# Performance work log

Hardware: AMD Instinct MI355X
Metric: run time of the kernel (lower is better)

The kernel has to match this reference:

```python
import jax, jax.numpy as jnp
import numpy as np

K_SIGMA = 4.0  # self.k in the torch module


def setup_inputs() -> dict:
    key = jax.random.key(0)
    k1, k2, k3 = jax.random.split(key, 3)
    B, N = 4096, 16384
    output = jax.random.normal(k1, (B, N), dtype=jnp.float32)
    mean_grad = jax.random.normal(k2, (N,), dtype=jnp.float32)
    var_grad = jax.random.uniform(k3, (N,), dtype=jnp.float32)  # variance >= 0
    return {"output": output, "mean_grad": mean_grad, "var_grad": var_grad}


def _nan_checker(x):
    # replace NaN/Inf with 0, matching nan_checker()
    return jnp.where(jnp.isnan(x) | jnp.isinf(x), jnp.zeros((), x.dtype), x)


def reference(output, mean_grad, var_grad):
    # circular conv1d with kernel [-1, 1, 0] == x[i] - x[i-1] (circular shift-sub)
    x = _nan_checker(output)                      # [B, N]
    grad_y = x - jnp.roll(x, 1, axis=1)           # [B, N]
    std = jnp.sqrt(var_grad)                      # [N]
    lower = mean_grad - K_SIGMA * std             # [N]
    upper = mean_grad + K_SIGMA * std             # [N]
    mask = (grad_y < lower) | (grad_y > upper)    # [B, N] outlier mask
    return jnp.where(mask, jnp.zeros((), x.dtype), x)
```

## Files before the change

### kernel.cpp

```cpp
#include <hip/hip_runtime.h>


#define N_COLS 16384
#define COLS4  (N_COLS / 4)
#define COLS4_SHIFT 12
#define COLS4_MASK  (COLS4 - 1)

__device__ __forceinline__ float nan_clean(float v) {
    unsigned u = __float_as_uint(v);
    return ((u & 0x7f800000u) == 0x7f800000u) ? 0.0f : v;
}

__global__ __launch_bounds__(256) void correction_kernel(
    const float* __restrict__ x,
    const float* __restrict__ mean_grad,
    const float* __restrict__ var_grad,
    float* __restrict__ out)
{
    int t = blockIdx.x * blockDim.x + threadIdx.x;
    int row  = t >> COLS4_SHIFT;
    int col4 = t & COLS4_MASK;
    int j    = col4 << 2;
    long base = (long)row * N_COLS + j;

    float4 x4 = *(const float4*)(x + base);
    int jprev = (j + N_COLS - 1) & (N_COLS - 1);
    float prev = x[(long)row * N_COLS + jprev];

    float c0 = nan_clean(x4.x);
    float c1 = nan_clean(x4.y);
    float c2 = nan_clean(x4.z);
    float c3 = nan_clean(x4.w);
    float cp = nan_clean(prev);

    float4 m4 = *(const float4*)(mean_grad + j);
    float4 v4 = *(const float4*)(var_grad + j);

    float s0 = 4.0f * sqrtf(v4.x);
    float s1 = 4.0f * sqrtf(v4.y);
    float s2 = 4.0f * sqrtf(v4.z);
    float s3 = 4.0f * sqrtf(v4.w);

    float d0 = c0 - cp;
    float d1 = c1 - c0;
    float d2 = c2 - c1;
    float d3 = c3 - c2;

    float4 o;
    o.x = (d0 < m4.x - s0 || d0 > m4.x + s0) ? 0.0f : c0;
    o.y = (d1 < m4.y - s1 || d1 > m4.y + s1) ? 0.0f : c1;
    o.z = (d2 < m4.z - s2 || d2 > m4.z + s2) ? 0.0f : c2;
    o.w = (d3 < m4.w - s3 || d3 > m4.w + s3) ? 0.0f : c3;

    *(float4*)(out + base) = o;
}

extern "C" void kernel_launch(void* const* d_in, const int* in_sizes, int n_in,
                              void* d_out, int out_size, void* d_ws, size_t ws_size,
                              hipStream_t stream) {
    const float* x  = (const float*)d_in[0];
    const float* mg = (const float*)d_in[1];
    const float* vg = (const float*)d_in[2];
    float* out = (float*)d_out;

    int B = in_sizes[0] / N_COLS;
    long total_threads = (long)B * COLS4;
    int block = 256;
    int grid = (int)((total_threads + block - 1) / block);

    correction_kernel<<<grid, block, 0, stream>>>(x, mg, vg, out);
}
```

Measured before the change: 421.5 us.

## Process 32 rows per block and reuse per-column bounds across rows

Switches to a 2D grid where each block covers 1024 columns and 32 rows. Each thread computes the lower and upper bounds (sqrt and scaling) once and applies them to 32 rows, with four independent row loads in flight per loop iteration. This drops repeated mean/var loads and sqrt work per element and adds memory-level parallelism. In exchange there are far fewer blocks (16x128), and B must be a multiple of 32.

```diff
diff --git a/kernel.cpp b/kernel.cpp
--- a/kernel.cpp
+++ b/kernel.cpp
@@ -2,13 +2,35 @@
 
 
 #define N_COLS 16384
-#define COLS4  (N_COLS / 4)
-#define COLS4_SHIFT 12
-#define COLS4_MASK  (COLS4 - 1)
+#define N_MASK (N_COLS - 1)
+#define COLS_PER_BLOCK 1024
+#define ROWS_PER_BLOCK 32
 
 __device__ __forceinline__ float nan_clean(float v) {
     unsigned u = __float_as_uint(v);
     return ((u & 0x7f800000u) == 0x7f800000u) ? 0.0f : v;
+}
+
+struct Bounds { float lo0, hi0, lo1, hi1, lo2, hi2, lo3, hi3; };
+
+__device__ __forceinline__ float4 correct4(float4 a, float p, const Bounds& b) {
+    float c0 = nan_clean(a.x);
+    float c1 = nan_clean(a.y);
+    float c2 = nan_clean(a.z);
+    float c3 = nan_clean(a.w);
+    float cp = nan_clean(p);
+
+    float d0 = c0 - cp;
+    float d1 = c1 - c0;
+    float d2 = c2 - c1;
+    float d3 = c3 - c2;
+
+    float4 o;
+    o.x = (d0 < b.lo0 || d0 > b.hi0) ? 0.0f : c0;
+    o.y = (d1 < b.lo1 || d1 > b.hi1) ? 0.0f : c1;
+    o.z = (d2 < b.lo2 || d2 > b.hi2) ? 0.0f : c2;
+    o.w = (d3 < b.lo3 || d3 > b.hi3) ? 0.0f : c3;
+    return o;
 }
 
 __global__ __launch_bounds__(256) void correction_kernel(
@@ -17,42 +39,40 @@
     const float* __restrict__ var_grad,
     float* __restrict__ out)
 {
-    int t = blockIdx.x * blockDim.x + threadIdx.x;
-    int row  = t >> COLS4_SHIFT;
-    int col4 = t & COLS4_MASK;
-    int j    = col4 << 2;
-    long base = (long)row * N_COLS + j;
+    const int c     = (blockIdx.x << 10) | (threadIdx.x << 2);
+    const int cprev = (c - 1) & N_MASK;
 
-    float4 x4 = *(const float4*)(x + base);
-    int jprev = (j + N_COLS - 1) & (N_COLS - 1);
-    float prev = x[(long)row * N_COLS + jprev];
+    float4 m4 = *(const float4*)(mean_grad + c);
+    float4 v4 = *(const float4*)(var_grad + c);
+    Bounds b;
+    float s;
+    s = 4.0f * sqrtf(v4.x); b.lo0 = m4.x - s; b.hi0 = m4.x + s;
+    s = 4.0f * sqrtf(v4.y); b.lo1 = m4.y - s; b.hi1 = m4.y + s;
+    s = 4.0f * sqrtf(v4.z); b.lo2 = m4.z - s; b.hi2 = m4.z + s;
+    s = 4.0f * sqrtf(v4.w); b.lo3 = m4.w - s; b.hi3 = m4.w + s;
 
-    float c0 = nan_clean(x4.x);
-    float c1 = nan_clean(x4.y);
-    float c2 = nan_clean(x4.z);
-    float c3 = nan_clean(x4.w);
-    float cp = nan_clean(prev);
+    const long rowbase = (long)blockIdx.y * ROWS_PER_BLOCK * N_COLS;
+    const float* xr = x + rowbase;
+    float*       orow = out + rowbase;
 
-    float4 m4 = *(const float4*)(mean_grad + j);
-    float4 v4 = *(const float4*)(var_grad + j);
+    for (int rr = 0; rr < ROWS_PER_BLOCK; rr += 4) {
+        float4 a0 = *(const float4*)(xr + c);
+        float  p0 = xr[cprev];
+        float4 a1 = *(const float4*)(xr + N_COLS + c);
+        float  p1 = xr[N_COLS + cprev];
+        float4 a2 = *(const float4*)(xr + 2 * N_COLS + c);
+        float  p2 = xr[2 * N_COLS + cprev];
+        float4 a3 = *(const float4*)(xr + 3 * N_COLS + c);
+        float  p3 = xr[3 * N_COLS + cprev];
 
-    float s0 = 4.0f * sqrtf(v4.x);
-    float s1 = 4.0f * sqrtf(v4.y);
-    float s2 = 4.0f * sqrtf(v4.z);
-    float s3 = 4.0f * sqrtf(v4.w);
+        *(float4*)(orow + c)              = correct4(a0, p0, b);
+        *(float4*)(orow + N_COLS + c)     = correct4(a1, p1, b);
+        *(float4*)(orow + 2 * N_COLS + c) = correct4(a2, p2, b);
+        *(float4*)(orow + 3 * N_COLS + c) = correct4(a3, p3, b);
 
-    float d0 = c0 - cp;
-    float d1 = c1 - c0;
-    float d2 = c2 - c1;
-    float d3 = c3 - c2;
-
-    float4 o;
-    o.x = (d0 < m4.x - s0 || d0 > m4.x + s0) ? 0.0f : c0;
-    o.y = (d1 < m4.y - s1 || d1 > m4.y + s1) ? 0.0f : c1;
-    o.z = (d2 < m4.z - s2 || d2 > m4.z + s2) ? 0.0f : c2;
-    o.w = (d3 < m4.w - s3 || d3 > m4.w + s3) ? 0.0f : c3;
-
-    *(float4*)(out + base) = o;
+        xr   += 4 * N_COLS;
+        orow += 4 * N_COLS;
+    }
 }
 
 extern "C" void kernel_launch(void* const* d_in, const int* in_sizes, int n_in,
@@ -64,9 +84,8 @@
     float* out = (float*)d_out;
 
     int B = in_sizes[0] / N_COLS;
-    long total_threads = (long)B * COLS4;
-    int block = 256;
-    int grid = (int)((total_threads + block - 1) / block);
+    dim3 grid(N_COLS / COLS_PER_BLOCK,
+              B / ROWS_PER_BLOCK);
 
-    correction_kernel<<<grid, block, 0, stream>>>(x, mg, vg, out);
+    correction_kernel<<<grid, dim3(256), 0, stream>>>(x, mg, vg, out);
 }
```

Result: slower. 448.3 us (+6.4%).
